# Performance work log

Hardware: AMD Instinct MI355X
Metric: run time of the kernel (lower is better)

Reference implementation:

```python
import jax, jax.numpy as jnp
import numpy as np

N = 50000      # nodes
E = 800000     # edges (avg degree 16)
IN = 128       # in_channels
OUT = 64       # out_channels
HID = 2 * OUT  # 128, hidden width of conv1
EPS = 1e-5     # BatchNorm eps


def _edge_norm(edge_index):
    # PyG ChebConv with sym normalization, lambda_max=2: L_hat = -D^{-1/2} A D^{-1/2}
    src, dst = edge_index[0], edge_index[1]
    deg = jax.ops.segment_sum(jnp.ones((E,), jnp.float32), src, num_segments=N)
    dinv = jnp.where(deg > 0, jax.lax.rsqrt(jnp.maximum(deg, 1.0)), 0.0)
    return -dinv[src] * dinv[dst]


def _cheb(x, src, dst, norm, W0, W1, b):
    # K=2 Chebyshev conv: Tx0 = x, Tx1 = L_hat x (sparse propagate)
    tx1 = jax.ops.segment_sum(x[src] * norm[:, None], dst, num_segments=N)
    return x @ W0 + tx1 @ W1 + b


def setup_inputs() -> dict:
    key = jax.random.key(0)
    ks = jax.random.split(key, 14)
    g = lambda k, shp, fan: jax.random.normal(k, shp, jnp.float32) / np.sqrt(fan)
    return {
        "x": jax.random.normal(ks[0], (N, IN), jnp.float32),
        "edge_index": jax.random.randint(ks[1], (2, E), 0, N, dtype=jnp.int32),
        "W1_0": g(ks[2], (IN, HID), IN),
        "W1_1": g(ks[3], (IN, HID), IN),
        "b1": jnp.zeros((HID,), jnp.float32),
        "gamma": jnp.ones((HID,), jnp.float32),
        "beta": jnp.zeros((HID,), jnp.float32),
        "Wmu_0": g(ks[4], (HID, OUT), HID),
        "Wmu_1": g(ks[5], (HID, OUT), HID),
        "b_mu": jnp.zeros((OUT,), jnp.float32),
        "Wls_0": g(ks[6], (HID, OUT), HID),
        "Wls_1": g(ks[7], (HID, OUT), HID),
        "b_ls": jnp.zeros((OUT,), jnp.float32),
    }


def reference(x, edge_index, W1_0, W1_1, b1, gamma, beta,
              Wmu_0, Wmu_1, b_mu, Wls_0, Wls_1, b_ls):
    src, dst = edge_index[0], edge_index[1]
    norm = _edge_norm(edge_index)
    h = _cheb(x, src, dst, norm, W1_0, W1_1, b1)         # [N, HID]
    # BatchNorm1d (training mode: batch statistics over nodes)
    mean = jnp.mean(h, axis=0)
    var = jnp.var(h, axis=0)
    h = (h - mean) * jax.lax.rsqrt(var + EPS) * gamma + beta
    h = jax.nn.relu(h)
    mu = _cheb(h, src, dst, norm, Wmu_0, Wmu_1, b_mu)    # [N, OUT]
    logstd = _cheb(h, src, dst, norm, Wls_0, Wls_1, b_ls)
    return (mu, logstd)
```

## Files before the change

kernel.cpp:

```cpp
#include <hip/hip_runtime.h>
#include <cstddef>
#include <cstdint>

static constexpr int IN_C  = 128;
static constexpr float BN_EPS = 1e-5f;
static constexpr int OUT_C = 64;

static constexpr int CS_C = 32;
static constexpr int CS_R = 8;
static constexpr int CS_RANGE = 6250;

using bf16x8 = __attribute__((ext_vector_type(8))) short;
using f32x4  = __attribute__((ext_vector_type(4))) float;

__device__ __forceinline__ ushort f2bf(float f) {
    uint u = __float_as_uint(f);
    u += 0x7fffu + ((u >> 16) & 1u);
    return (ushort)(u >> 16);
}
__device__ __forceinline__ uint pack2(float a, float b) {
    return (uint)f2bf(a) | ((uint)f2bf(b) << 16);
}
__device__ __forceinline__ float bf_lo(uint v) { return __uint_as_float(v << 16); }
__device__ __forceinline__ float bf_hi(uint v) { return __uint_as_float(v & 0xffff0000u); }

__device__ __forceinline__ int swz8(int row, int g) { return (g ^ ((row >> 1) & 3)) * 8; }

__global__ __launch_bounds__(1024) void hist_k(
    const int* __restrict__ src, const int* __restrict__ dst,
    int* __restrict__ hsrc_part, int* __restrict__ hdst_part,
    int N, int E, int chunk, int range) {
    __shared__ int hs_[CS_RANGE];
    __shared__ int hd_[CS_RANGE];
    int c = blockIdx.x & (CS_C - 1);
    int r = blockIdx.x / CS_C;
    int base = r * range;
    int hi = min(base + range, N);
    int rsz = hi - base;
    for (int j = threadIdx.x; j < rsz; j += 1024) { hs_[j] = 0; hd_[j] = 0; }
    __syncthreads();
    int e0 = c * chunk, e1 = min(e0 + chunk, E);
    for (int i = e0 + threadIdx.x; i < e1; i += 1024) {
        int s = src[i];
        if (s >= base && s < hi) atomicAdd(&hs_[s - base], 1);
        int t = dst[i];
        if (t >= base && t < hi) atomicAdd(&hd_[t - base], 1);
    }
    __syncthreads();
    for (int j = threadIdx.x; j < rsz; j += 1024) {
        hsrc_part[(size_t)c * N + base + j] = hs_[j];
        hdst_part[(size_t)c * N + base + j] = hd_[j];
    }
}

__global__ __launch_bounds__(256) void count_k(
    const int* __restrict__ hsrc_part, const int* __restrict__ hdst_part,
    float* __restrict__ dinv, int* __restrict__ cnt_dst,
    int* __restrict__ bsum, float* __restrict__ stats, int N) {
    __shared__ int sw[4];
    int tid = threadIdx.x;
    if (blockIdx.x == 0) stats[tid] = 0.f;
    int v = blockIdx.x * 256 + tid;
    int b = 0;
    if (v < N) {
        int a = 0;
        for (int c = 0; c < CS_C; ++c) {
            a += hsrc_part[(size_t)c * N + v];
            b += hdst_part[(size_t)c * N + v];
        }
        dinv[v] = (a > 0) ? rsqrtf((float)a) : 0.f;
        cnt_dst[v] = b;
    }
    int t = b;
    #pragma unroll
    for (int off = 1; off < 64; off <<= 1) t += __shfl_xor(t, off, 64);
    if ((tid & 63) == 0) sw[tid >> 6] = t;
    __syncthreads();
    if (tid == 0) bsum[blockIdx.x] = sw[0] + sw[1] + sw[2] + sw[3];
}

__global__ __launch_bounds__(256) void bscan_k(int* __restrict__ bsum, int nb) {
    __shared__ int sm[256];
    int tid = threadIdx.x;
    int v = (tid < nb) ? bsum[tid] : 0;
    sm[tid] = v;
    __syncthreads();
    #pragma unroll
    for (int off = 1; off < 256; off <<= 1) {
        int t = (tid >= off) ? sm[tid - off] : 0;
        __syncthreads();
        sm[tid] += t;
        __syncthreads();
    }
    if (tid < nb) bsum[tid] = sm[tid] - v;
}

__global__ __launch_bounds__(256) void phase3_k(
    const int* __restrict__ cnt, const int* __restrict__ bsum,
    int* __restrict__ row_ptr, int* __restrict__ hdst_part, int n) {
    __shared__ int swv[4];
    int tid = threadIdx.x;
    int lane = tid & 63, wave = tid >> 6;
    int v = blockIdx.x * 256 + tid;
    int c = (v < n) ? cnt[v] : 0;
    int s = c;
    #pragma unroll
    for (int off = 1; off < 64; off <<= 1) {
        int t = __shfl_up(s, off, 64);
        if (lane >= off) s += t;
    }
    if (lane == 63) swv[wave] = s;
    __syncthreads();
    int wexcl = 0;
    for (int w = 0; w < wave; ++w) wexcl += swv[w];
    int st = bsum[blockIdx.x] + wexcl + (s - c);
    if (v < n) row_ptr[v + 1] = st + c;
    if (v == 0) row_ptr[0] = 0;
    int r = st;
    for (int ch = 0; ch < CS_C; ++ch) {
        size_t idx = (size_t)ch * n + v;
        if (v < n) {
            int t = hdst_part[idx];
            hdst_part[idx] = r;
            r += t;
        }
    }
}

__global__ __launch_bounds__(1024) void scatter_k(
    const int* __restrict__ src, const int* __restrict__ dst,
    const int* __restrict__ off, int* __restrict__ col,
    int N, int E, int chunk, int range) {
    __shared__ int cur[CS_RANGE];
    int c = blockIdx.x & (CS_C - 1);
    int r = blockIdx.x / CS_C;
    int base = r * range;
    int hi = min(base + range, N);
    int rsz = hi - base;
    for (int j = threadIdx.x; j < rsz; j += 1024)
        cur[j] = off[(size_t)c * N + base + j];
    __syncthreads();
    int e0 = c * chunk, e1 = min(e0 + chunk, E);
    for (int i = e0 + threadIdx.x; i < e1; i += 1024) {
        int t = dst[i];
        if (t >= base && t < hi) {
            int pos = atomicAdd(&cur[t - base], 1);
            col[pos] = src[i];
        }
    }
}

__global__ void convert_prep_k(const float* __restrict__ in, const float* __restrict__ dinv,
                               ushort* __restrict__ xb, ushort* __restrict__ xsb, int n64,
                               int nb_conv,
                               const float* __restrict__ W1_0, const float* __restrict__ W1_1,
                               const float* __restrict__ b1,
                               const float* __restrict__ Wmu_0, const float* __restrict__ Wmu_1,
                               const float* __restrict__ b_mu,
                               const float* __restrict__ Wls_0, const float* __restrict__ Wls_1,
                               const float* __restrict__ b_ls,
                               ushort* __restrict__ Wt1, ushort* __restrict__ Wt2,
                               float* __restrict__ bias1, float* __restrict__ bias2) {
    int bid = blockIdx.x;
    if (bid < nb_conv) {
        int i = bid * 256 + threadIdx.x;
        if (i >= n64) return;
        int row = i >> 6;
        float d = dinv[row];
        float2 v = ((const float2*)in)[i];
        ((uint*)xb)[i] = pack2(v.x, v.y);
        ((uint*)xsb)[i] = pack2(v.x * d, v.y * d);
    } else {
        int idx = (bid - nb_conv) * 256 + threadIdx.x;
        int which = idx >> 15;
        int c = (idx >> 8) & 127;
        int k = idx & 255;
        if (which == 0) {
            float v = (k < 128) ? W1_0[k * 128 + c] : W1_1[(k - 128) * 128 + c];
            Wt1[c * 256 + k] = f2bf(v);
            if (k == 0) bias1[c] = b1[c];
        } else {
            float v;
            if (c < 64) v = (k < 128) ? Wmu_0[k * 64 + c] : Wmu_1[(k - 128) * 64 + c];
            else        v = (k < 128) ? Wls_0[k * 64 + (c - 64)] : Wls_1[(k - 128) * 64 + (c - 64)];
            Wt2[c * 256 + k] = f2bf(v);
            if (k == 0) bias2[c] = (c < 64) ? b_mu[c] : b_ls[c - 64];
        }
    }
}

#define ACC8(V)                                         \
    acc[0] += bf_lo((V).x); acc[1] += bf_hi((V).x);     \
    acc[2] += bf_lo((V).y); acc[3] += bf_hi((V).y);     \
    acc[4] += bf_lo((V).z); acc[5] += bf_hi((V).z);     \
    acc[6] += bf_lo((V).w); acc[7] += bf_hi((V).w);

__global__ __launch_bounds__(256) void propagate4_k(
    const uint4* __restrict__ xs, uint4* __restrict__ out,
    const int* __restrict__ row_ptr, const int* __restrict__ col,
    const float* __restrict__ dinv, int n) {
    int wid = (blockIdx.x * 256 + threadIdx.x) >> 6;
    if (wid >= n) return;
    int lane = threadIdx.x & 63;
    int g = lane >> 4, li = lane & 15;
    int s = row_ptr[wid], e = row_ptr[wid + 1];
    float acc[8];
    #pragma unroll
    for (int k = 0; k < 8; ++k) acc[k] = 0.f;
    int i = s + g;
    for (; i + 12 < e; i += 16) {
        int c0 = col[i];
        int c1 = col[i + 4];
        int c2 = col[i + 8];
        int c3 = col[i + 12];
        uint4 v0 = xs[(size_t)c0 * 16 + li];
        uint4 v1 = xs[(size_t)c1 * 16 + li];
        uint4 v2 = xs[(size_t)c2 * 16 + li];
        uint4 v3 = xs[(size_t)c3 * 16 + li];
        ACC8(v0); ACC8(v1); ACC8(v2); ACC8(v3);
    }
    for (; i < e; i += 4) {
        int c0 = col[i];
        uint4 v0 = xs[(size_t)c0 * 16 + li];
        ACC8(v0);
    }
    #pragma unroll
    for (int k = 0; k < 8; ++k) {
        acc[k] += __shfl_xor(acc[k], 16, 64);
        acc[k] += __shfl_xor(acc[k], 32, 64);
    }
    if (g == 0) {
        float sc = -dinv[wid];
        uint4 o;
        o.x = pack2(acc[0] * sc, acc[1] * sc);
        o.y = pack2(acc[2] * sc, acc[3] * sc);
        o.z = pack2(acc[4] * sc, acc[5] * sc);
        o.w = pack2(acc[6] * sc, acc[7] * sc);
        out[(size_t)wid * 16 + li] = o;
    }
}

template <int MODE>
__global__ __launch_bounds__(256) void gemm_mfma_k(
    const ushort* __restrict__ A0, const ushort* __restrict__ A1,
    const ushort* __restrict__ Wt, const float* __restrict__ bias,
    ushort* __restrict__ Cb, float* __restrict__ Cmu, float* __restrict__ Cls,
    float* __restrict__ stats, int n) {
    __shared__ ushort sA[64][32];
    __shared__ ushort sW[128][32];
    __shared__ float smS[4][128];
    __shared__ float smQ[4][128];

    int tid = threadIdx.x;
    int block_row = blockIdx.x * 64;
    int wave = tid >> 6, lane = tid & 63;
    int col_base = lane & 15;
    int quad = lane >> 4;
    int m_local = wave * 16 + col_base;

    f32x4 acc[8];
    #pragma unroll
    for (int t = 0; t < 8; ++t) acc[t] = (f32x4){0.f, 0.f, 0.f, 0.f};

    for (int k0 = 0; k0 < 256; k0 += 32) {
        {
            int row = tid >> 2, g = tid & 3;
            int grow = block_row + row;
            int kc = k0 + g * 8;
            uint4 v = make_uint4(0, 0, 0, 0);
            if (grow < n) {
                const ushort* srcp = (kc < 128) ? (A0 + (size_t)grow * 128 + kc)
                                                : (A1 + (size_t)grow * 128 + (kc - 128));
                v = *(const uint4*)srcp;
            }
            *(uint4*)&sA[row][swz8(row, g)] = v;
        }
        #pragma unroll
        for (int i = tid; i < 512; i += 256) {
            int c = i >> 2, g = i & 3;
            *(uint4*)&sW[c][swz8(c, g)] = *(const uint4*)(Wt + (size_t)c * 256 + k0 + g * 8);
        }
        __syncthreads();
        bf16x8 af = *(const bf16x8*)&sA[m_local][swz8(m_local, quad)];
        #pragma unroll
        for (int t = 0; t < 8; ++t) {
            int wr = t * 16 + col_base;
            bf16x8 bfr = *(const bf16x8*)&sW[wr][swz8(wr, quad)];
            acc[t] = __builtin_amdgcn_mfma_f32_16x16x32_bf16(af, bfr, acc[t], 0, 0, 0);
        }
        __syncthreads();
    }

    int row_l = wave * 16 + quad * 4;
    #pragma unroll
    for (int t = 0; t < 8; ++t) {
        int col = t * 16 + col_base;
        float b = bias[col];
        float s = 0.f, q = 0.f;
        #pragma unroll
        for (int r = 0; r < 4; ++r) {
            int grow = block_row + row_l + r;
            if (grow < n) {
                float v = acc[t][r] + b;
                if (MODE == 0) {
                    Cb[(size_t)grow * 128 + col] = f2bf(v);
                    s += v; q += v * v;
                } else {
                    if (col < 64) Cmu[(size_t)grow * 64 + col] = v;
                    else          Cls[(size_t)grow * 64 + (col - 64)] = v;
                }
            }
        }
        if (MODE == 0) {
            s += __shfl_xor(s, 16, 64); s += __shfl_xor(s, 32, 64);
            q += __shfl_xor(q, 16, 64); q += __shfl_xor(q, 32, 64);
            if (quad == 0) { smS[wave][col] = s; smQ[wave][col] = q; }
        }
    }
    if (MODE == 0) {
        __syncthreads();
        if (tid < 128) {
            float s = smS[0][tid] + smS[1][tid] + smS[2][tid] + smS[3][tid];
            float q = smQ[0][tid] + smQ[1][tid] + smQ[2][tid] + smQ[3][tid];
            atomicAdd(&stats[tid], s);
            atomicAdd(&stats[128 + tid], q);
        }
    }
}

__global__ __launch_bounds__(256) void bn_apply_k(
    ushort* __restrict__ hb, ushort* __restrict__ hsb,
    const float* __restrict__ stats, const float* __restrict__ gamma,
    const float* __restrict__ beta, const float* __restrict__ dinv,
    float inv_n, int n64) {
    __shared__ float sp[256];
    int tid = threadIdx.x;
    if (tid < 128) {
        float mean = stats[tid] * inv_n;
        float var = stats[128 + tid] * inv_n - mean * mean;
        float sc = gamma[tid] * rsqrtf(var + BN_EPS);
        sp[tid] = sc;
        sp[128 + tid] = beta[tid] - mean * sc;
    }
    __syncthreads();
    int i = blockIdx.x * 256 + tid;
    if (i >= n64) return;
    int c2 = (i & 63) * 2;
    int row = i >> 6;
    uint v = ((uint*)hb)[i];
    float f0 = fmaxf(bf_lo(v) * sp[c2]     + sp[128 + c2],     0.f);
    float f1 = fmaxf(bf_hi(v) * sp[c2 + 1] + sp[128 + c2 + 1], 0.f);
    ((uint*)hb)[i] = pack2(f0, f1);
    float d = dinv[row];
    ((uint*)hsb)[i] = pack2(f0 * d, f1 * d);
}

extern "C" void kernel_launch(void* const* d_in, const int* in_sizes, int n_in,
                              void* d_out, int out_size, void* d_ws, size_t ws_size,
                              hipStream_t stream) {
    const float* x = (const float*)d_in[0];
    const int* edge_index = (const int*)d_in[1];
    const float* W1_0 = (const float*)d_in[2];
    const float* W1_1 = (const float*)d_in[3];
    const float* b1 = (const float*)d_in[4];
    const float* gamma = (const float*)d_in[5];
    const float* beta = (const float*)d_in[6];
    const float* Wmu_0 = (const float*)d_in[7];
    const float* Wmu_1 = (const float*)d_in[8];
    const float* b_mu = (const float*)d_in[9];
    const float* Wls_0 = (const float*)d_in[10];
    const float* Wls_1 = (const float*)d_in[11];
    const float* b_ls = (const float*)d_in[12];

    const int N = in_sizes[0] / IN_C;
    const int E = in_sizes[1] / 2;
    const int* src = edge_index;
    const int* dst = edge_index + E;

    char* w = (char*)d_ws;
    auto alloc = [&](size_t bytes) {
        char* p = w;
        w += (bytes + 15) & ~(size_t)15;
        return p;
    };
    float* stats = (float*)alloc(256 * 4);
    int* row_ptr = (int*)alloc((size_t)(N + 1) * 4);
    int* bsum    = (int*)alloc(256 * 4);
    float* dinv  = (float*)alloc((size_t)N * 4);
    int* cnt_dst = (int*)alloc((size_t)N * 4);
    int* col     = (int*)alloc((size_t)E * 4);
    int* hsrc_part = (int*)alloc((size_t)CS_C * N * 4);
    int* hdst_part = (int*)alloc((size_t)CS_C * N * 4);
    ushort* x_bf  = (ushort*)alloc((size_t)N * 128 * 2);
    ushort* xs_bf = (ushort*)alloc((size_t)N * 128 * 2);
    ushort* xp_bf = (ushort*)alloc((size_t)N * 128 * 2);
    ushort* h_bf  = (ushort*)alloc((size_t)N * 128 * 2);
    ushort* Wt1   = (ushort*)alloc(128 * 256 * 2);
    ushort* Wt2   = (ushort*)alloc(128 * 256 * 2);
    float* bias1  = (float*)alloc(128 * 4);
    float* bias2  = (float*)alloc(128 * 4);

    ushort* hs_bf = xs_bf;
    ushort* hp_bf = xp_bf;

    float* out_mu = (float*)d_out;
    float* out_ls = out_mu + (size_t)N * OUT_C;

    int chunk = (E + CS_C - 1) / CS_C;
    int range = (N + CS_R - 1) / CS_R;
    int NBLK = (N + 255) / 256;
    int nb_conv = (N * 64 + 255) / 256;

    hist_k<<<CS_R * CS_C, 1024, 0, stream>>>(src, dst, hsrc_part, hdst_part, N, E, chunk, range);
    count_k<<<NBLK, 256, 0, stream>>>(hsrc_part, hdst_part, dinv, cnt_dst, bsum, stats, N);
    bscan_k<<<1, 256, 0, stream>>>(bsum, NBLK);
    phase3_k<<<NBLK, 256, 0, stream>>>(cnt_dst, bsum, row_ptr, hdst_part, N);
    scatter_k<<<CS_R * CS_C, 1024, 0, stream>>>(src, dst, hdst_part, col, N, E, chunk, range);

    convert_prep_k<<<nb_conv + 256, 256, 0, stream>>>(
        x, dinv, x_bf, xs_bf, N * 64, nb_conv,
        W1_0, W1_1, b1, Wmu_0, Wmu_1, b_mu, Wls_0, Wls_1, b_ls,
        Wt1, Wt2, bias1, bias2);

    int pb = (N + 3) / 4;
    propagate4_k<<<pb, 256, 0, stream>>>((const uint4*)xs_bf, (uint4*)xp_bf,
                                         row_ptr, col, dinv, N);

    int gb = (N + 63) / 64;
    gemm_mfma_k<0><<<gb, 256, 0, stream>>>(x_bf, xp_bf, Wt1, bias1, h_bf,
                                           nullptr, nullptr, stats, N);

    bn_apply_k<<<(N * 64 + 255) / 256, 256, 0, stream>>>(h_bf, hs_bf, stats, gamma, beta,
                                                         dinv, 1.f / (float)N, N * 64);

    propagate4_k<<<pb, 256, 0, stream>>>((const uint4*)hs_bf, (uint4*)hp_bf,
                                         row_ptr, col, dinv, N);

    gemm_mfma_k<1><<<gb, 256, 0, stream>>>(h_bf, hp_bf, Wt2, bias2, nullptr,
                                           out_mu, out_ls, stats, N);
}
```

Before: 291.2 us.

## Fuse sparse propagation into MFMA GEMM and fold block scan into phase3

The separate propagate kernel is merged into the GEMM kernel. Each block first gathers neighbor rows for its 64 nodes into shared memory, then uses that tile as the second half of K, so the intermediate propagated buffer no longer makes a global round trip. The single-block bscan launch is also removed: each phase3 block reduces the preceding block sums itself. The cost is lower parallelism in the gather (one wave processes 16 rows in sequence with 782 blocks) and more shared memory per block, which may reduce occupancy and latency hiding.

```diff
diff --git a/kernel.cpp b/kernel.cpp
--- a/kernel.cpp
+++ b/kernel.cpp
@@ -79,28 +79,23 @@
     if (tid == 0) bsum[blockIdx.x] = sw[0] + sw[1] + sw[2] + sw[3];
 }
 
-__global__ __launch_bounds__(256) void bscan_k(int* __restrict__ bsum, int nb) {
-    __shared__ int sm[256];
-    int tid = threadIdx.x;
-    int v = (tid < nb) ? bsum[tid] : 0;
-    sm[tid] = v;
-    __syncthreads();
-    #pragma unroll
-    for (int off = 1; off < 256; off <<= 1) {
-        int t = (tid >= off) ? sm[tid - off] : 0;
-        __syncthreads();
-        sm[tid] += t;
-        __syncthreads();
-    }
-    if (tid < nb) bsum[tid] = sm[tid] - v;
-}
-
 __global__ __launch_bounds__(256) void phase3_k(
     const int* __restrict__ cnt, const int* __restrict__ bsum,
-    int* __restrict__ row_ptr, int* __restrict__ hdst_part, int n) {
+    int* __restrict__ row_ptr, int* __restrict__ hdst_part, int n, int nb) {
+    __shared__ int swp[4];
     __shared__ int swv[4];
+    __shared__ int sbase;
     int tid = threadIdx.x;
     int lane = tid & 63, wave = tid >> 6;
+    int pv = (tid < nb && tid < (int)blockIdx.x) ? bsum[tid] : 0;
+    int ps = pv;
+    #pragma unroll
+    for (int off = 1; off < 64; off <<= 1) ps += __shfl_xor(ps, off, 64);
+    if (lane == 0) swp[wave] = ps;
+    __syncthreads();
+    if (tid == 0) sbase = swp[0] + swp[1] + swp[2] + swp[3];
+    __syncthreads();
+
     int v = blockIdx.x * 256 + tid;
     int c = (v < n) ? cnt[v] : 0;
     int s = c;
@@ -113,7 +108,7 @@
     __syncthreads();
     int wexcl = 0;
     for (int w = 0; w < wave; ++w) wexcl += swv[w];
-    int st = bsum[blockIdx.x] + wexcl + (s - c);
+    int st = sbase + wexcl + (s - c);
     if (v < n) row_ptr[v + 1] = st + c;
     if (v == 0) row_ptr[0] = 0;
     int r = st;
@@ -195,57 +190,15 @@
     acc[4] += bf_lo((V).z); acc[5] += bf_hi((V).z);     \
     acc[6] += bf_lo((V).w); acc[7] += bf_hi((V).w);
 
-__global__ __launch_bounds__(256) void propagate4_k(
-    const uint4* __restrict__ xs, uint4* __restrict__ out,
+template <int MODE>
+__global__ __launch_bounds__(256) void conv_fused_k(
+    const ushort* __restrict__ A0, const uint4* __restrict__ xs,
     const int* __restrict__ row_ptr, const int* __restrict__ col,
-    const float* __restrict__ dinv, int n) {
-    int wid = (blockIdx.x * 256 + threadIdx.x) >> 6;
-    if (wid >= n) return;
-    int lane = threadIdx.x & 63;
-    int g = lane >> 4, li = lane & 15;
-    int s = row_ptr[wid], e = row_ptr[wid + 1];
-    float acc[8];
-    #pragma unroll
-    for (int k = 0; k < 8; ++k) acc[k] = 0.f;
-    int i = s + g;
-    for (; i + 12 < e; i += 16) {
-        int c0 = col[i];
-        int c1 = col[i + 4];
-        int c2 = col[i + 8];
-        int c3 = col[i + 12];
-        uint4 v0 = xs[(size_t)c0 * 16 + li];
-        uint4 v1 = xs[(size_t)c1 * 16 + li];
-        uint4 v2 = xs[(size_t)c2 * 16 + li];
-        uint4 v3 = xs[(size_t)c3 * 16 + li];
-        ACC8(v0); ACC8(v1); ACC8(v2); ACC8(v3);
-    }
-    for (; i < e; i += 4) {
-        int c0 = col[i];
-        uint4 v0 = xs[(size_t)c0 * 16 + li];
-        ACC8(v0);
-    }
-    #pragma unroll
-    for (int k = 0; k < 8; ++k) {
-        acc[k] += __shfl_xor(acc[k], 16, 64);
-        acc[k] += __shfl_xor(acc[k], 32, 64);
-    }
-    if (g == 0) {
-        float sc = -dinv[wid];
-        uint4 o;
-        o.x = pack2(acc[0] * sc, acc[1] * sc);
-        o.y = pack2(acc[2] * sc, acc[3] * sc);
-        o.z = pack2(acc[4] * sc, acc[5] * sc);
-        o.w = pack2(acc[6] * sc, acc[7] * sc);
-        out[(size_t)wid * 16 + li] = o;
-    }
-}
-
-template <int MODE>
-__global__ __launch_bounds__(256) void gemm_mfma_k(
-    const ushort* __restrict__ A0, const ushort* __restrict__ A1,
+    const float* __restrict__ dinv,
     const ushort* __restrict__ Wt, const float* __restrict__ bias,
     ushort* __restrict__ Cb, float* __restrict__ Cmu, float* __restrict__ Cls,
     float* __restrict__ stats, int n) {
+    __shared__ ushort sP[4][64][32];
     __shared__ ushort sA[64][32];
     __shared__ ushort sW[128][32];
     __shared__ float smS[4][128];
@@ -254,67 +207,110 @@
     int tid = threadIdx.x;
     int block_row = blockIdx.x * 64;
     int wave = tid >> 6, lane = tid & 63;
-    int col_base = lane & 15;
-    int quad = lane >> 4;
-    int m_local = wave * 16 + col_base;
-
-    f32x4 acc[8];
+    int g = lane >> 4, li = lane & 15;
+
+    #pragma unroll 1
+    for (int t = 0; t < 16; ++t) {
+        int ln = wave * 16 + t;
+        int gr = block_row + ln;
+        float acc[8];
+        #pragma unroll
+        for (int k = 0; k < 8; ++k) acc[k] = 0.f;
+        if (gr < n) {
+            int s = row_ptr[gr], e = row_ptr[gr + 1];
+            int i = s + g;
+            #pragma unroll 1
+            for (; i + 12 < e; i += 16) {
+                int c0 = col[i];
+                int c1 = col[i + 4];
+                int c2 = col[i + 8];
+                int c3 = col[i + 12];
+                uint4 v0 = xs[(size_t)c0 * 16 + li];
+                uint4 v1 = xs[(size_t)c1 * 16 + li];
+                uint4 v2 = xs[(size_t)c2 * 16 + li];
+                uint4 v3 = xs[(size_t)c3 * 16 + li];
+                ACC8(v0); ACC8(v1); ACC8(v2); ACC8(v3);
+            }
+            #pragma unroll 1
+            for (; i < e; i += 4) {
+                int c0 = col[i];
+                uint4 v0 = xs[(size_t)c0 * 16 + li];
+                ACC8(v0);
+            }
+        }
+        #pragma unroll
+        for (int k = 0; k < 8; ++k) {
+            acc[k] += __shfl_xor(acc[k], 16, 64);
+            acc[k] += __shfl_xor(acc[k], 32, 64);
+        }
+        if (g == 0) {
+            float sc = (gr < n) ? -dinv[gr] : 0.f;
+            uint4 o;
+            o.x = pack2(acc[0] * sc, acc[1] * sc);
+            o.y = pack2(acc[2] * sc, acc[3] * sc);
+            o.z = pack2(acc[4] * sc, acc[5] * sc);
+            o.w = pack2(acc[6] * sc, acc[7] * sc);
+            *(uint4*)&sP[li >> 2][ln][swz8(ln, li & 3)] = o;
+        }
+    }
+    __syncthreads();
+
+    int m_local = wave * 16 + li;
+    f32x4 accm[8];
     #pragma unroll
-    for (int t = 0; t < 8; ++t) acc[t] = (f32x4){0.f, 0.f, 0.f, 0.f};
-
+    for (int t = 0; t < 8; ++t) accm[t] = (f32x4){0.f, 0.f, 0.f, 0.f};
+
+    #pragma unroll 1
     for (int k0 = 0; k0 < 256; k0 += 32) {
-        {
-            int row = tid >> 2, g = tid & 3;
+        int kp = k0 >> 5;
+        if (kp < 4) {
+            int row = tid >> 2, gg = tid & 3;
             int grow = block_row + row;
-            int kc = k0 + g * 8;
             uint4 v = make_uint4(0, 0, 0, 0);
-            if (grow < n) {
-                const ushort* srcp = (kc < 128) ? (A0 + (size_t)grow * 128 + kc)
-                                                : (A1 + (size_t)grow * 128 + (kc - 128));
-                v = *(const uint4*)srcp;
-            }
-            *(uint4*)&sA[row][swz8(row, g)] = v;
+            if (grow < n) v = *(const uint4*)(A0 + (size_t)grow * 128 + k0 + gg * 8);
+            *(uint4*)&sA[row][swz8(row, gg)] = v;
         }
         #pragma unroll
         for (int i = tid; i < 512; i += 256) {
-            int c = i >> 2, g = i & 3;
-            *(uint4*)&sW[c][swz8(c, g)] = *(const uint4*)(Wt + (size_t)c * 256 + k0 + g * 8);
+            int cc = i >> 2, gg = i & 3;
+            *(uint4*)&sW[cc][swz8(cc, gg)] = *(const uint4*)(Wt + (size_t)cc * 256 + k0 + gg * 8);
         }
         __syncthreads();
-        bf16x8 af = *(const bf16x8*)&sA[m_local][swz8(m_local, quad)];
+        bf16x8 af = (kp < 4) ? *(const bf16x8*)&sA[m_local][swz8(m_local, g)]
+                             : *(const bf16x8*)&sP[kp - 4][m_local][swz8(m_local, g)];
         #pragma unroll
         for (int t = 0; t < 8; ++t) {
-            int wr = t * 16 + col_base;
-            bf16x8 bfr = *(const bf16x8*)&sW[wr][swz8(wr, quad)];
-            acc[t] = __builtin_amdgcn_mfma_f32_16x16x32_bf16(af, bfr, acc[t], 0, 0, 0);
+            int wr = t * 16 + li;
+            bf16x8 bfr = *(const bf16x8*)&sW[wr][swz8(wr, g)];
+            accm[t] = __builtin_amdgcn_mfma_f32_16x16x32_bf16(af, bfr, accm[t], 0, 0, 0);
         }
         __syncthreads();
     }
 
-    int row_l = wave * 16 + quad * 4;
-    #pragma unroll
+    int row_l = wave * 16 + g * 4;
+    #pragma unroll 1
     for (int t = 0; t < 8; ++t) {
-        int col = t * 16 + col_base;
-        float b = bias[col];
+        int cc = t * 16 + li;
+        float b = bias[cc];
         float s = 0.f, q = 0.f;
         #pragma unroll
         for (int r = 0; r < 4; ++r) {
             int grow = block_row + row_l + r;
             if (grow < n) {
-                float v = acc[t][r] + b;
+                float v = accm[t][r] + b;
                 if (MODE == 0) {
-                    Cb[(size_t)grow * 128 + col] = f2bf(v);
+                    Cb[(size_t)grow * 128 + cc] = f2bf(v);
                     s += v; q += v * v;
                 } else {
-                    if (col < 64) Cmu[(size_t)grow * 64 + col] = v;
-                    else          Cls[(size_t)grow * 64 + (col - 64)] = v;
+                    if (cc < 64) Cmu[(size_t)grow * 64 + cc] = v;
+                    else         Cls[(size_t)grow * 64 + (cc - 64)] = v;
                 }
             }
         }
         if (MODE == 0) {
             s += __shfl_xor(s, 16, 64); s += __shfl_xor(s, 32, 64);
             q += __shfl_xor(q, 16, 64); q += __shfl_xor(q, 32, 64);
-            if (quad == 0) { smS[wave][col] = s; smQ[wave][col] = q; }
+            if (g == 0) { smS[wave][cc] = s; smQ[wave][cc] = q; }
         }
     }
     if (MODE == 0) {
@@ -393,7 +389,6 @@
     int* hdst_part = (int*)alloc((size_t)CS_C * N * 4);
     ushort* x_bf  = (ushort*)alloc((size_t)N * 128 * 2);
     ushort* xs_bf = (ushort*)alloc((size_t)N * 128 * 2);
-    ushort* xp_bf = (ushort*)alloc((size_t)N * 128 * 2);
     ushort* h_bf  = (ushort*)alloc((size_t)N * 128 * 2);
     ushort* Wt1   = (ushort*)alloc(128 * 256 * 2);
     ushort* Wt2   = (ushort*)alloc(128 * 256 * 2);
@@ -401,7 +396,6 @@
     float* bias2  = (float*)alloc(128 * 4);
 
     ushort* hs_bf = xs_bf;
-    ushort* hp_bf = xp_bf;
 
     float* out_mu = (float*)d_out;
     float* out_ls = out_mu + (size_t)N * OUT_C;
@@ -413,8 +407,7 @@
 
     hist_k<<<CS_R * CS_C, 1024, 0, stream>>>(src, dst, hsrc_part, hdst_part, N, E, chunk, range);
     count_k<<<NBLK, 256, 0, stream>>>(hsrc_part, hdst_part, dinv, cnt_dst, bsum, stats, N);
-    bscan_k<<<1, 256, 0, stream>>>(bsum, NBLK);
-    phase3_k<<<NBLK, 256, 0, stream>>>(cnt_dst, bsum, row_ptr, hdst_part, N);
+    phase3_k<<<NBLK, 256, 0, stream>>>(cnt_dst, bsum, row_ptr, hdst_part, N, NBLK);
     scatter_k<<<CS_R * CS_C, 1024, 0, stream>>>(src, dst, hdst_part, col, N, E, chunk, range);
 
     convert_prep_k<<<nb_conv + 256, 256, 0, stream>>>(
@@ -422,20 +415,13 @@
         W1_0, W1_1, b1, Wmu_0, Wmu_1, b_mu, Wls_0, Wls_1, b_ls,
         Wt1, Wt2, bias1, bias2);
 
-    int pb = (N + 3) / 4;
-    propagate4_k<<<pb, 256, 0, stream>>>((const uint4*)xs_bf, (uint4*)xp_bf,
-                                         row_ptr, col, dinv, N);
-
     int gb = (N + 63) / 64;
-    gemm_mfma_k<0><<<gb, 256, 0, stream>>>(x_bf, xp_bf, Wt1, bias1, h_bf,
-                                           nullptr, nullptr, stats, N);
+    conv_fused_k<0><<<gb, 256, 0, stream>>>(x_bf, (const uint4*)xs_bf, row_ptr, col, dinv,
+                                            Wt1, bias1, h_bf, nullptr, nullptr, stats, N);
 
     bn_apply_k<<<(N * 64 + 255) / 256, 256, 0, stream>>>(h_bf, hs_bf, stats, gamma, beta,
                                                          dinv, 1.f / (float)N, N * 64);
 
-    propagate4_k<<<pb, 256, 0, stream>>>((const uint4*)hs_bf, (uint4*)hp_bf,
-                                         row_ptr, col, dinv, N);
-
-    gemm_mfma_k<1><<<gb, 256, 0, stream>>>(h_bf, hp_bf, Wt2, bias2, nullptr,
-                                           out_mu, out_ls, stats, N);
-}
+    conv_fused_k<1><<<gb, 256, 0, stream>>>(h_bf, (const uint4*)hs_bf, row_ptr, col, dinv,
+                                            Wt2, bias2, nullptr, out_mu, out_ls, stats, N);
+}
```

Measured after the change: 308.3 us. 5.9% more time.
